# Kernel optimization log

Hardware: AMD Instinct MI355X
Metric: run time of the kernel (lower is better)

## Reference

```python
import jax, jax.numpy as jnp
import numpy as np

NUM_HEADS = 8
DEPTH_K = 256
DEPTH_V = 256


def rel_to_abs(x):
    # x: [B, Nh, L, 2L-1] -> [B, Nh, L, L] via the pad/reshape skew trick
    B, Nh, L, _ = x.shape
    x = jnp.pad(x, ((0, 0), (0, 0), (0, 0), (0, 1)))            # [B,Nh,L,2L]
    flat = x.reshape(B, Nh, L * 2 * L)
    flat = jnp.pad(flat, ((0, 0), (0, 0), (0, L - 1)))
    final = flat.reshape(B, Nh, L + 1, 2 * L - 1)
    return final[:, :, :L, L - 1:]


def relative_logits_1d(q, rel_k, H, W, transpose_mask):
    # q: [B, Nh, H, W, d]; rel_k: [2W-1, d]
    B, Nh = q.shape[0], q.shape[1]
    rel = jnp.einsum('bhxyd,md->bhxym', q, rel_k)               # [B,Nh,H,W,2W-1]
    rel = rel.reshape(B, Nh * H, W, 2 * W - 1)
    rel = rel_to_abs(rel)                                       # [B,Nh*H,W,W]
    rel = rel.reshape(B, Nh, H, W, W)
    rel = jnp.broadcast_to(rel[:, :, :, None, :, :], (B, Nh, H, H, W, W))
    rel = jnp.transpose(rel, transpose_mask)
    return rel.reshape(B, Nh, H * W, H * W)


def split_heads_2d(x):
    B, H, W, c = x.shape
    x = x.reshape(B, H, W, NUM_HEADS, c // NUM_HEADS)
    return jnp.transpose(x, (0, 3, 1, 2, 4))                     # [B,Nh,H,W,d]


def setup_inputs() -> dict:
    key = jax.random.key(0)
    k1, k2, k3 = jax.random.split(key, 3)
    dk_head = DEPTH_K // NUM_HEADS
    H = W = 32
    inputs = jax.random.normal(k1, (8, H, W, 2 * DEPTH_K + DEPTH_V), dtype=jnp.float32)
    key_rel_w = jax.random.normal(k2, (2 * W - 1, dk_head), dtype=jnp.float32) * dk_head ** -0.5
    key_rel_h = jax.random.normal(k3, (2 * H - 1, dk_head), dtype=jnp.float32) * dk_head ** -0.5
    return {"inputs": inputs, "key_rel_w": key_rel_w, "key_rel_h": key_rel_h}


def reference(inputs, key_rel_w, key_rel_h):
    B, H, W, _ = inputs.shape
    q, k, v = jnp.split(inputs, [DEPTH_K, 2 * DEPTH_K], axis=-1)
    q = split_heads_2d(q) * (DEPTH_K / NUM_HEADS) ** -0.5        # [B,Nh,H,W,dk]
    k = split_heads_2d(k)
    v = split_heads_2d(v)

    flat_q = q.reshape(B, NUM_HEADS, H * W, -1)
    flat_k = k.reshape(B, NUM_HEADS, H * W, -1)
    flat_v = v.reshape(B, NUM_HEADS, H * W, -1)

    logits = jnp.einsum('bnqd,bnkd->bnqk', flat_q, flat_k)       # [B,Nh,HW,HW]
    w_rel = relative_logits_1d(q, key_rel_w, H, W, (0, 1, 2, 4, 3, 5))
    h_rel = relative_logits_1d(jnp.transpose(q, (0, 1, 3, 2, 4)), key_rel_h,
                               W, H, (0, 1, 4, 2, 5, 3))
    logits = logits + h_rel + w_rel

    weights = jax.nn.softmax(logits, axis=-1)
    attn = jnp.einsum('bnqk,bnkd->bnqd', weights, flat_v)        # [B,Nh,HW,dv]
    attn = attn.reshape(B, NUM_HEADS, H, W, -1)
    out = jnp.transpose(attn, (0, 2, 3, 1, 4)).reshape(B, H, W, DEPTH_V)
    return out
```

## Files before the change

kernel.cpp:

```cpp
#include <hip/hip_runtime.h>
#include <hip/hip_bf16.h>

typedef short bf16x8 __attribute__((ext_vector_type(8)));
typedef float f32x4  __attribute__((ext_vector_type(4)));

#define DEVINL static __device__ __forceinline__

DEVINL unsigned short f2bf(float x){
  union { float f; unsigned u; } v; v.f = x;
  unsigned r = v.u + 0x7fffu + ((v.u >> 16) & 1u);
  return (unsigned short)(r >> 16);
}
DEVINL float bf2f(unsigned short b){
  union { unsigned u; float f; } v; v.u = ((unsigned)b) << 16; return v.f;
}
DEVINL unsigned pk2(float a, float b){
  __hip_bfloat162 h = __float22bfloat162_rn(float2{a, b});
  union { __hip_bfloat162 h2; unsigned u; } cv; cv.h2 = h; return cv.u;
}

__global__ __launch_bounds__(256, 2)
void aug_attn_kernel(const float* __restrict__ inp,
                     const float* __restrict__ relw,
                     const float* __restrict__ relh,
                     float* __restrict__ out)
{
  __shared__ __align__(16) unsigned short s_rw[128*66];
  __shared__ __align__(16) unsigned short s_rh[128*34];
  __shared__ __align__(16) unsigned short s_k [2][64*40];
  __shared__ __align__(16) unsigned short s_vt[2][32*72];
  __shared__ __align__(16) unsigned short s_p [4][32*72];

  const int tid  = threadIdx.x;
  const int wv   = tid >> 6;
  const int lane = tid & 63;
  const int lo16 = lane & 15;
  const int hi4  = lane >> 4;

  const int bid = blockIdx.x;
  const int bn  = bid >> 3;
  const int qc  = bid & 7;
  const int b   = bn >> 3;
  const int n   = bn & 7;
  const int x1  = qc*4 + wv;

  const float qscale = 0.17677669529663687f;
  const float L2E    = 1.44269504088896f;
  const float MFIX   = 8.0f;

  const int krow = tid >> 2;
  const int c8   = (tid & 3)*8;
  const float* kptr = inp + ((size_t)(b*1024 + krow))*768 + 256 + n*32 + c8;
  const float* vptr = kptr + 256;
  const size_t kstep = (size_t)64*768;

  float4 kA = *(const float4*)kptr;
  float4 kB = *(const float4*)(kptr+4);
  float4 vA = *(const float4*)vptr;
  float4 vB = *(const float4*)(vptr+4);

  bf16x8 qf[2];
#pragma unroll
  for (int qt=0; qt<2; ++qt){
    const float* qp = inp + ((size_t)((b*32 + x1)*32 + qt*16 + lo16))*768 + n*32 + hi4*8;
    float4 a = *(const float4*)qp;
    float4 c = *(const float4*)(qp+4);
    union { unsigned u[4]; bf16x8 v; } cv;
    cv.u[0]=pk2(a.x*qscale, a.y*qscale);
    cv.u[1]=pk2(a.z*qscale, a.w*qscale);
    cv.u[2]=pk2(c.x*qscale, c.y*qscale);
    cv.u[3]=pk2(c.z*qscale, c.w*qscale);
    qf[qt] = cv.v;
  }

#pragma unroll
  for (int mt=0; mt<4; ++mt){
    const int m = mt*16 + lo16;
    bf16x8 rf = {0,0,0,0,0,0,0,0};
    if (m < 63){
      const float* rp = relw + m*32 + hi4*8;
      float4 a = *(const float4*)rp;
      float4 c = *(const float4*)(rp+4);
      union { unsigned u[4]; bf16x8 v; } cv;
      cv.u[0]=pk2(a.x,a.y); cv.u[1]=pk2(a.z,a.w);
      cv.u[2]=pk2(c.x,c.y); cv.u[3]=pk2(c.z,c.w);
      rf = cv.v;
    }
#pragma unroll
    for (int qt=0; qt<2; ++qt){
      f32x4 acc = {0.f,0.f,0.f,0.f};
      acc = __builtin_amdgcn_mfma_f32_16x16x32_bf16(qf[qt], rf, acc, 0,0,0);
      const int qrow = wv*32 + qt*16 + hi4*4;
#pragma unroll
      for (int r=0;r<4;++r)
        s_rw[(qrow+r)*66 + m] = f2bf(acc[r]);
    }
  }

#pragma unroll
  for (int mt=0; mt<4; ++mt){
    const int m = mt*16 + lo16;
    bf16x8 rf = {0,0,0,0,0,0,0,0};
    if (m < 63){
      const float* rp = relh + m*32 + hi4*8;
      float4 a = *(const float4*)rp;
      float4 c = *(const float4*)(rp+4);
      union { unsigned u[4]; bf16x8 v; } cv;
      cv.u[0]=pk2(a.x,a.y); cv.u[1]=pk2(a.z,a.w);
      cv.u[2]=pk2(c.x,c.y); cv.u[3]=pk2(c.z,c.w);
      rf = cv.v;
    }
    const int x2 = m + x1 - 31;
#pragma unroll
    for (int qt=0; qt<2; ++qt){
      f32x4 acc = {0.f,0.f,0.f,0.f};
      acc = __builtin_amdgcn_mfma_f32_16x16x32_bf16(qf[qt], rf, acc, 0,0,0);
      const int qrow = wv*32 + qt*16 + hi4*4;
      if (x2 >= 0 && x2 < 32){
#pragma unroll
        for (int r=0;r<4;++r)
          s_rh[(qrow+r)*34 + x2] = f2bf(acc[r]);
      }
    }
  }

  float rwl2[2][2][4];
#pragma unroll
  for (int qt=0; qt<2; ++qt){
    const int y1q  = qt*16 + lo16;
    const int qrow = wv*32 + y1q;
    const int mb   = 31 - y1q + 4*hi4;
#pragma unroll
    for (int p=0;p<2;++p)
#pragma unroll
      for (int r=0;r<4;++r)
        rwl2[qt][p][r] = (bf2f(s_rw[qrow*66 + mb + 16*p + r]) - MFIX)*L2E;
  }

  float l_run[2] = {0.f, 0.f};
  f32x4 accO[2][2];
#pragma unroll
  for (int qt=0;qt<2;++qt)
#pragma unroll
    for (int dvt=0;dvt<2;++dvt){
      f32x4 z = {0.f,0.f,0.f,0.f};
      accO[qt][dvt] = z;
    }

  unsigned short* pbuf = s_p[wv];

  for (int kb=0; kb<16; ++kb){
    const int cur = kb & 1;
    {
      uint4 kw; kw.x=pk2(kA.x,kA.y); kw.y=pk2(kA.z,kA.w);
                kw.z=pk2(kB.x,kB.y); kw.w=pk2(kB.z,kB.w);
      *(uint4*)(&s_k[cur][krow*40 + c8]) = kw;
      unsigned v0=pk2(vA.x,vA.y), v1=pk2(vA.z,vA.w);
      unsigned v2=pk2(vB.x,vB.y), v3=pk2(vB.z,vB.w);
      unsigned short* vt = s_vt[cur];
      vt[(c8+0)*72 + krow] = (unsigned short)(v0);
      vt[(c8+1)*72 + krow] = (unsigned short)(v0>>16);
      vt[(c8+2)*72 + krow] = (unsigned short)(v1);
      vt[(c8+3)*72 + krow] = (unsigned short)(v1>>16);
      vt[(c8+4)*72 + krow] = (unsigned short)(v2);
      vt[(c8+5)*72 + krow] = (unsigned short)(v2>>16);
      vt[(c8+6)*72 + krow] = (unsigned short)(v3);
      vt[(c8+7)*72 + krow] = (unsigned short)(v3>>16);
    }
    __syncthreads();

    if (kb < 15){
      kptr += kstep; vptr += kstep;
      kA = *(const float4*)kptr;
      kB = *(const float4*)(kptr+4);
      vA = *(const float4*)vptr;
      vB = *(const float4*)(vptr+4);
    }

    bf16x8 kfrag[4];
#pragma unroll
    for (int kt=0;kt<4;++kt)
      kfrag[kt] = *(const bf16x8*)(&s_k[cur][(kt*16 + lo16)*40 + hi4*8]);

    f32x4 S[2][4];
#pragma unroll
    for (int qt=0;qt<2;++qt)
#pragma unroll
      for (int kt=0;kt<4;++kt){
        f32x4 z = {0.f,0.f,0.f,0.f};
        S[qt][kt] = __builtin_amdgcn_mfma_f32_16x16x32_bf16(kfrag[kt], qf[qt], z, 0,0,0);
      }

#pragma unroll
    for (int qt=0;qt<2;++qt){
      const int y1   = qt*16 + lo16;
      const int qrow = wv*32 + y1;
      const unsigned rhu = *(const unsigned*)(&s_rh[qrow*34 + 2*kb]);
      const float rh0L = bf2f((unsigned short)(rhu & 0xffffu))*L2E;
      const float rh1L = bf2f((unsigned short)(rhu >> 16))*L2E;
      float lacc = 0.f;
#pragma unroll
      for (int kt=0;kt<4;++kt){
        const float rhL = (kt<2)? rh0L : rh1L;
        const int p = kt & 1;
        float pv[4];
#pragma unroll
        for (int r=0;r<4;++r)
          pv[r] = exp2f(__builtin_fmaf(S[qt][kt][r], L2E, rwl2[qt][p][r] + rhL));
        lacc += (pv[0]+pv[1]) + (pv[2]+pv[3]);
        unsigned* d32 = (unsigned*)(pbuf + y1*72 + kt*16 + hi4*4);
        d32[0] = pk2(pv[0], pv[1]);
        d32[1] = pk2(pv[2], pv[3]);
      }
      l_run[qt] += lacc;
    }

    bf16x8 vfrag[2][2];
#pragma unroll
    for (int dvt=0;dvt<2;++dvt)
#pragma unroll
      for (int kc=0;kc<2;++kc)
        vfrag[dvt][kc] = *(const bf16x8*)(&s_vt[cur][(dvt*16+lo16)*72 + kc*32 + hi4*8]);
#pragma unroll
    for (int qt=0;qt<2;++qt)
#pragma unroll
      for (int kc=0;kc<2;++kc){
        bf16x8 pfrag = *(const bf16x8*)(&pbuf[(qt*16+lo16)*72 + kc*32 + hi4*8]);
#pragma unroll
        for (int dvt=0;dvt<2;++dvt)
          accO[qt][dvt] = __builtin_amdgcn_mfma_f32_16x16x32_bf16(
                            vfrag[dvt][kc], pfrag, accO[qt][dvt], 0,0,0);
      }
  }

#pragma unroll
  for (int qt=0;qt<2;++qt){
    float l = l_run[qt];
    l += __shfl_xor(l, 16, 64);
    l += __shfl_xor(l, 32, 64);
    const float inv = 1.f / l;
    const int y1 = qt*16 + lo16;
    float* op = out + ((size_t)((b*32 + x1)*32 + y1))*256 + n*32;
#pragma unroll
    for (int dvt=0;dvt<2;++dvt){
      float4 o;
      o.x = accO[qt][dvt][0]*inv;
      o.y = accO[qt][dvt][1]*inv;
      o.z = accO[qt][dvt][2]*inv;
      o.w = accO[qt][dvt][3]*inv;
      *(float4*)(op + dvt*16 + hi4*4) = o;
    }
  }
}

extern "C" void kernel_launch(void* const* d_in, const int* in_sizes, int n_in,
                              void* d_out, int out_size, void* d_ws, size_t ws_size,
                              hipStream_t stream) {
  (void)in_sizes; (void)n_in; (void)d_ws; (void)ws_size; (void)out_size;
  const float* inp  = (const float*)d_in[0];
  const float* relw = (const float*)d_in[1];
  const float* relh = (const float*)d_in[2];
  float* out = (float*)d_out;
  dim3 grid(512), block(256);
  aug_attn_kernel<<<grid, block, 0, stream>>>(inp, relw, relh, out);
}
```

Baseline: 105.7 us.

## Split query tiles across 8 waves and keep P in registers via permlane swaps

```diff
diff --git a/kernel.cpp b/kernel.cpp
--- a/kernel.cpp
+++ b/kernel.cpp
@@ -3,6 +3,7 @@
 
 typedef short bf16x8 __attribute__((ext_vector_type(8)));
 typedef float f32x4  __attribute__((ext_vector_type(4)));
+typedef unsigned uintx2 __attribute__((ext_vector_type(2)));
 
 #define DEVINL static __device__ __forceinline__
 
@@ -18,8 +19,11 @@
   __hip_bfloat162 h = __float22bfloat162_rn(float2{a, b});
   union { __hip_bfloat162 h2; unsigned u; } cv; cv.h2 = h; return cv.u;
 }
-
-__global__ __launch_bounds__(256, 2)
+DEVINL float fexp2(float x){
+  float r; asm("v_exp_f32 %0, %1" : "=v"(r) : "v"(x)); return r;
+}
+
+__global__ __launch_bounds__(512, 4)
 void aug_attn_kernel(const float* __restrict__ inp,
                      const float* __restrict__ relw,
                      const float* __restrict__ relh,
@@ -28,8 +32,7 @@
   __shared__ __align__(16) unsigned short s_rw[128*66];
   __shared__ __align__(16) unsigned short s_rh[128*34];
   __shared__ __align__(16) unsigned short s_k [2][64*40];
-  __shared__ __align__(16) unsigned short s_vt[2][32*72];
-  __shared__ __align__(16) unsigned short s_p [4][32*72];
+  __shared__ __align__(16) unsigned short s_vt[2][32*64];
 
   const int tid  = threadIdx.x;
   const int wv   = tid >> 6;
@@ -42,27 +45,35 @@
   const int qc  = bid & 7;
   const int b   = bn >> 3;
   const int n   = bn & 7;
-  const int x1  = qc*4 + wv;
+  const int x1l = wv >> 1;
+  const int qh  = wv & 1;
+  const int x1  = qc*4 + x1l;
+  const int y1  = qh*16 + lo16;
+  const int qrow = x1l*32 + y1;
 
   const float qscale = 0.17677669529663687f;
   const float L2E    = 1.44269504088896f;
   const float MFIX   = 8.0f;
 
-  const int krow = tid >> 2;
-  const int c8   = (tid & 3)*8;
-  const float* kptr = inp + ((size_t)(b*1024 + krow))*768 + 256 + n*32 + c8;
+  const int krow = tid >> 3;
+  const int c4   = (tid & 7) << 2;
+  const float* kptr = inp + ((size_t)(b*1024 + krow))*768 + 256 + n*32 + c4;
   const float* vptr = kptr + 256;
   const size_t kstep = (size_t)64*768;
 
   float4 kA = *(const float4*)kptr;
-  float4 kB = *(const float4*)(kptr+4);
   float4 vA = *(const float4*)vptr;
-  float4 vB = *(const float4*)(vptr+4);
-
-  bf16x8 qf[2];
-#pragma unroll
-  for (int qt=0; qt<2; ++qt){
-    const float* qp = inp + ((size_t)((b*32 + x1)*32 + qt*16 + lo16))*768 + n*32 + hi4*8;
+
+  int vslot[4];
+#pragma unroll
+  for (int j=0;j<4;++j){
+    const int dv = c4 + j;
+    vslot[j] = dv*64 + ((((krow>>3) ^ (dv&7) ^ ((dv>>3)&3)))<<3) + (krow&7);
+  }
+
+  bf16x8 qf;
+  {
+    const float* qp = inp + ((size_t)((b*32 + x1)*32 + y1))*768 + n*32 + hi4*8;
     float4 a = *(const float4*)qp;
     float4 c = *(const float4*)(qp+4);
     union { unsigned u[4]; bf16x8 v; } cv;
@@ -70,7 +81,7 @@
     cv.u[1]=pk2(a.z*qscale, a.w*qscale);
     cv.u[2]=pk2(c.x*qscale, c.y*qscale);
     cv.u[3]=pk2(c.z*qscale, c.w*qscale);
-    qf[qt] = cv.v;
+    qf = cv.v;
   }
 
 #pragma unroll
@@ -86,15 +97,12 @@
       cv.u[2]=pk2(c.x,c.y); cv.u[3]=pk2(c.z,c.w);
       rf = cv.v;
     }
-#pragma unroll
-    for (int qt=0; qt<2; ++qt){
-      f32x4 acc = {0.f,0.f,0.f,0.f};
-      acc = __builtin_amdgcn_mfma_f32_16x16x32_bf16(qf[qt], rf, acc, 0,0,0);
-      const int qrow = wv*32 + qt*16 + hi4*4;
-#pragma unroll
-      for (int r=0;r<4;++r)
-        s_rw[(qrow+r)*66 + m] = f2bf(acc[r]);
-    }
+    f32x4 acc = {0.f,0.f,0.f,0.f};
+    acc = __builtin_amdgcn_mfma_f32_16x16x32_bf16(qf, rf, acc, 0,0,0);
+    const int rw0 = x1l*32 + qh*16 + hi4*4;
+#pragma unroll
+    for (int r=0;r<4;++r)
+      s_rw[(rw0+r)*66 + m] = f2bf(acc[r]);
   }
 
 #pragma unroll
@@ -111,70 +119,51 @@
       rf = cv.v;
     }
     const int x2 = m + x1 - 31;
-#pragma unroll
-    for (int qt=0; qt<2; ++qt){
-      f32x4 acc = {0.f,0.f,0.f,0.f};
-      acc = __builtin_amdgcn_mfma_f32_16x16x32_bf16(qf[qt], rf, acc, 0,0,0);
-      const int qrow = wv*32 + qt*16 + hi4*4;
-      if (x2 >= 0 && x2 < 32){
-#pragma unroll
-        for (int r=0;r<4;++r)
-          s_rh[(qrow+r)*34 + x2] = f2bf(acc[r]);
-      }
-    }
-  }
-
-  float rwl2[2][2][4];
-#pragma unroll
-  for (int qt=0; qt<2; ++qt){
-    const int y1q  = qt*16 + lo16;
-    const int qrow = wv*32 + y1q;
-    const int mb   = 31 - y1q + 4*hi4;
+    f32x4 acc = {0.f,0.f,0.f,0.f};
+    acc = __builtin_amdgcn_mfma_f32_16x16x32_bf16(qf, rf, acc, 0,0,0);
+    if (x2 >= 0 && x2 < 32){
+      const int rw0 = x1l*32 + qh*16 + hi4*4;
+#pragma unroll
+      for (int r=0;r<4;++r)
+        s_rh[(rw0+r)*34 + x2] = f2bf(acc[r]);
+    }
+  }
+
+  float rwl2[2][4];
+  {
+    const int mb = 31 - y1 + 4*hi4;
 #pragma unroll
     for (int p=0;p<2;++p)
 #pragma unroll
       for (int r=0;r<4;++r)
-        rwl2[qt][p][r] = (bf2f(s_rw[qrow*66 + mb + 16*p + r]) - MFIX)*L2E;
-  }
-
-  float l_run[2] = {0.f, 0.f};
-  f32x4 accO[2][2];
-#pragma unroll
-  for (int qt=0;qt<2;++qt)
-#pragma unroll
-    for (int dvt=0;dvt<2;++dvt){
-      f32x4 z = {0.f,0.f,0.f,0.f};
-      accO[qt][dvt] = z;
-    }
-
-  unsigned short* pbuf = s_p[wv];
+        rwl2[p][r] = (bf2f(s_rw[qrow*66 + mb + 16*p + r]) - MFIX)*L2E;
+  }
+
+  float l_run = 0.f;
+  f32x4 accO[2];
+  {
+    f32x4 z = {0.f,0.f,0.f,0.f};
+    accO[0] = z; accO[1] = z;
+  }
 
   for (int kb=0; kb<16; ++kb){
     const int cur = kb & 1;
     {
-      uint4 kw; kw.x=pk2(kA.x,kA.y); kw.y=pk2(kA.z,kA.w);
-                kw.z=pk2(kB.x,kB.y); kw.w=pk2(kB.z,kB.w);
-      *(uint4*)(&s_k[cur][krow*40 + c8]) = kw;
-      unsigned v0=pk2(vA.x,vA.y), v1=pk2(vA.z,vA.w);
-      unsigned v2=pk2(vB.x,vB.y), v3=pk2(vB.z,vB.w);
+      uintx2 kw; kw[0]=pk2(kA.x,kA.y); kw[1]=pk2(kA.z,kA.w);
+      *(uintx2*)(&s_k[cur][krow*40 + c4]) = kw;
+      const unsigned u0 = pk2(vA.x, vA.y), u1 = pk2(vA.z, vA.w);
       unsigned short* vt = s_vt[cur];
-      vt[(c8+0)*72 + krow] = (unsigned short)(v0);
-      vt[(c8+1)*72 + krow] = (unsigned short)(v0>>16);
-      vt[(c8+2)*72 + krow] = (unsigned short)(v1);
-      vt[(c8+3)*72 + krow] = (unsigned short)(v1>>16);
-      vt[(c8+4)*72 + krow] = (unsigned short)(v2);
-      vt[(c8+5)*72 + krow] = (unsigned short)(v2>>16);
-      vt[(c8+6)*72 + krow] = (unsigned short)(v3);
-      vt[(c8+7)*72 + krow] = (unsigned short)(v3>>16);
+      vt[vslot[0]] = (unsigned short)u0;
+      vt[vslot[1]] = (unsigned short)(u0>>16);
+      vt[vslot[2]] = (unsigned short)u1;
+      vt[vslot[3]] = (unsigned short)(u1>>16);
     }
     __syncthreads();
 
     if (kb < 15){
       kptr += kstep; vptr += kstep;
       kA = *(const float4*)kptr;
-      kB = *(const float4*)(kptr+4);
       vA = *(const float4*)vptr;
-      vB = *(const float4*)(vptr+4);
     }
 
     bf16x8 kfrag[4];
@@ -182,74 +171,79 @@
     for (int kt=0;kt<4;++kt)
       kfrag[kt] = *(const bf16x8*)(&s_k[cur][(kt*16 + lo16)*40 + hi4*8]);
 
-    f32x4 S[2][4];
-#pragma unroll
-    for (int qt=0;qt<2;++qt)
-#pragma unroll
-      for (int kt=0;kt<4;++kt){
-        f32x4 z = {0.f,0.f,0.f,0.f};
-        S[qt][kt] = __builtin_amdgcn_mfma_f32_16x16x32_bf16(kfrag[kt], qf[qt], z, 0,0,0);
+    bf16x8 vfrag[2][2];
+#pragma unroll
+    for (int dvt=0;dvt<2;++dvt){
+      const int dv = dvt*16 + lo16;
+      const int xr = (dv&7) ^ ((dv>>3)&3);
+#pragma unroll
+      for (int kc=0;kc<2;++kc){
+        const int blk = (kc*4 + hi4) ^ xr;
+        vfrag[dvt][kc] = *(const bf16x8*)(&s_vt[cur][dv*64 + blk*8]);
       }
-
-#pragma unroll
-    for (int qt=0;qt<2;++qt){
-      const int y1   = qt*16 + lo16;
-      const int qrow = wv*32 + y1;
-      const unsigned rhu = *(const unsigned*)(&s_rh[qrow*34 + 2*kb]);
-      const float rh0L = bf2f((unsigned short)(rhu & 0xffffu))*L2E;
-      const float rh1L = bf2f((unsigned short)(rhu >> 16))*L2E;
-      float lacc = 0.f;
-#pragma unroll
-      for (int kt=0;kt<4;++kt){
-        const float rhL = (kt<2)? rh0L : rh1L;
-        const int p = kt & 1;
-        float pv[4];
-#pragma unroll
-        for (int r=0;r<4;++r)
-          pv[r] = exp2f(__builtin_fmaf(S[qt][kt][r], L2E, rwl2[qt][p][r] + rhL));
-        lacc += (pv[0]+pv[1]) + (pv[2]+pv[3]);
-        unsigned* d32 = (unsigned*)(pbuf + y1*72 + kt*16 + hi4*4);
-        d32[0] = pk2(pv[0], pv[1]);
-        d32[1] = pk2(pv[2], pv[3]);
-      }
-      l_run[qt] += lacc;
-    }
-
-    bf16x8 vfrag[2][2];
-#pragma unroll
-    for (int dvt=0;dvt<2;++dvt)
-#pragma unroll
-      for (int kc=0;kc<2;++kc)
-        vfrag[dvt][kc] = *(const bf16x8*)(&s_vt[cur][(dvt*16+lo16)*72 + kc*32 + hi4*8]);
-#pragma unroll
-    for (int qt=0;qt<2;++qt)
-#pragma unroll
-      for (int kc=0;kc<2;++kc){
-        bf16x8 pfrag = *(const bf16x8*)(&pbuf[(qt*16+lo16)*72 + kc*32 + hi4*8]);
-#pragma unroll
-        for (int dvt=0;dvt<2;++dvt)
-          accO[qt][dvt] = __builtin_amdgcn_mfma_f32_16x16x32_bf16(
-                            vfrag[dvt][kc], pfrag, accO[qt][dvt], 0,0,0);
-      }
-  }
-
-#pragma unroll
-  for (int qt=0;qt<2;++qt){
-    float l = l_run[qt];
-    l += __shfl_xor(l, 16, 64);
-    l += __shfl_xor(l, 32, 64);
-    const float inv = 1.f / l;
-    const int y1 = qt*16 + lo16;
-    float* op = out + ((size_t)((b*32 + x1)*32 + y1))*256 + n*32;
-#pragma unroll
-    for (int dvt=0;dvt<2;++dvt){
-      float4 o;
-      o.x = accO[qt][dvt][0]*inv;
-      o.y = accO[qt][dvt][1]*inv;
-      o.z = accO[qt][dvt][2]*inv;
-      o.w = accO[qt][dvt][3]*inv;
-      *(float4*)(op + dvt*16 + hi4*4) = o;
-    }
+    }
+
+    f32x4 S[4];
+#pragma unroll
+    for (int kt=0;kt<4;++kt){
+      f32x4 z = {0.f,0.f,0.f,0.f};
+      S[kt] = __builtin_amdgcn_mfma_f32_16x16x32_bf16(kfrag[kt], qf, z, 0,0,0);
+    }
+
+    const unsigned rhu = *(const unsigned*)(&s_rh[qrow*34 + 2*kb]);
+    const float rh0L = bf2f((unsigned short)(rhu & 0xffffu))*L2E;
+    const float rh1L = bf2f((unsigned short)(rhu >> 16))*L2E;
+    unsigned W[4][2];
+    float lacc = 0.f;
+#pragma unroll
+    for (int kt=0;kt<4;++kt){
+      const float rhL = (kt<2)? rh0L : rh1L;
+      const int p = kt & 1;
+      float pv0 = fexp2(__builtin_fmaf(S[kt][0], L2E, rwl2[p][0] + rhL));
+      float pv1 = fexp2(__builtin_fmaf(S[kt][1], L2E, rwl2[p][1] + rhL));
+      float pv2 = fexp2(__builtin_fmaf(S[kt][2], L2E, rwl2[p][2] + rhL));
+      float pv3 = fexp2(__builtin_fmaf(S[kt][3], L2E, rwl2[p][3] + rhL));
+      lacc += (pv0+pv1) + (pv2+pv3);
+      W[kt][0] = pk2(pv0, pv1);
+      W[kt][1] = pk2(pv2, pv3);
+    }
+    l_run += lacc;
+
+    bf16x8 pfrag[2];
+#pragma unroll
+    for (int kc=0;kc<2;++kc){
+      unsigned r0 = W[2*kc][0],   r1 = W[2*kc][1];
+      unsigned r2 = W[2*kc+1][0], r3 = W[2*kc+1][1];
+      asm("v_permlane32_swap_b32 %0, %1" : "+v"(r0), "+v"(r2));
+      asm("v_permlane32_swap_b32 %0, %1" : "+v"(r1), "+v"(r3));
+      asm("v_permlane16_swap_b32 %0, %1" : "+v"(r0), "+v"(r2));
+      asm("v_permlane16_swap_b32 %0, %1" : "+v"(r1), "+v"(r3));
+      union { unsigned u[4]; bf16x8 v; } cv;
+      cv.u[0]=r0; cv.u[1]=r1; cv.u[2]=r2; cv.u[3]=r3;
+      pfrag[kc] = cv.v;
+    }
+
+#pragma unroll
+    for (int kc=0;kc<2;++kc)
+#pragma unroll
+      for (int dvt=0;dvt<2;++dvt)
+        accO[dvt] = __builtin_amdgcn_mfma_f32_16x16x32_bf16(
+                      vfrag[dvt][kc], pfrag[kc], accO[dvt], 0,0,0);
+  }
+
+  float l = l_run;
+  l += __shfl_xor(l, 16, 64);
+  l += __shfl_xor(l, 32, 64);
+  const float inv = 1.f / l;
+  float* op = out + ((size_t)((b*32 + x1)*32 + y1))*256 + n*32;
+#pragma unroll
+  for (int dvt=0;dvt<2;++dvt){
+    float4 o;
+    o.x = accO[dvt][0]*inv;
+    o.y = accO[dvt][1]*inv;
+    o.z = accO[dvt][2]*inv;
+    o.w = accO[dvt][3]*inv;
+    *(float4*)(op + dvt*16 + hi4*4) = o;
   }
 }
 
@@ -261,6 +255,6 @@
   const float* relw = (const float*)d_in[1];
   const float* relh = (const float*)d_in[2];
   float* out = (float*)d_out;
-  dim3 grid(512), block(256);
+  dim3 grid(512), block(512);
   aug_attn_kernel<<<grid, block, 0, stream>>>(inp, relw, relh, out);
 }
```

Result: faster. 102.1 us (-3.4%).
